# Kernel optimization log

Measured on AMD Instinct MI355X. Metric: run time of the kernel, lower is better.

The kernel has to match this reference:

```python
import jax, jax.numpy as jnp
import numpy as np

PAD = 0          # pad_token_id == blank_index in the source module
NEG = -1e30      # log-space 'zero' (safe for fp32)


def _ctc_mean_loss(labels, logits, logits_mask):
    """Faithful jnp port of CTCLoss.call: tf.nn.ctc_loss (alpha forward DP,
    blank=pad, dense labels, logits [B,T,V]) + feasibility mask + mean."""
    B, T, V = logits.shape
    L = labels.shape[1]
    S = 2 * L + 1

    labels_len = jnp.sum(labels != PAD, axis=-1).astype(jnp.int32)   # [B]
    logits_len = jnp.sum(logits_mask, axis=-1).astype(jnp.int32)     # [B]

    logp = jax.nn.log_softmax(logits.astype(jnp.float32), axis=-1)   # [B,T,V]

    # Blank-interleaved extended label sequence: (blank, l1, blank, l2, ..., blank)
    ext = jnp.full((B, S), PAD, dtype=labels.dtype)
    ext = ext.at[:, 1::2].set(labels)                                # [B,S]
    ext_m2 = jnp.pad(ext, ((0, 0), (2, 0)), constant_values=PAD)[:, :S]
    allow_skip = (ext != PAD) & (ext != ext_m2)                      # [B,S]

    # Emission log-probs gathered at extended labels: em[b,t,s] = logp[b,t,ext[b,s]]
    em = jnp.take_along_axis(logp, jnp.broadcast_to(ext[:, None, :], (B, T, S)), axis=2)
    em = em.transpose(1, 0, 2)                                       # [T,B,S]

    neg = jnp.float32(NEG)
    alpha0 = jnp.full((B, S), neg, dtype=jnp.float32)
    alpha0 = alpha0.at[:, 0].set(em[0, :, 0]).at[:, 1].set(em[0, :, 1])

    t_idx = jnp.arange(1, T, dtype=jnp.int32)
    active = t_idx[:, None] < logits_len[None, :]                    # [T-1,B]

    def step(alpha, inp):
        em_t, act = inp                                              # [B,S], [B]
        p1 = jnp.concatenate([jnp.full((B, 1), neg), alpha[:, :-1]], axis=1)
        p2 = jnp.concatenate([jnp.full((B, 2), neg), alpha[:, :-2]], axis=1)
        p2 = jnp.where(allow_skip, p2, neg)
        new = em_t + jnp.logaddexp(jnp.logaddexp(alpha, p1), p2)
        alpha = jnp.where(act[:, None], new, alpha)                  # freeze past logit_len
        return alpha, None

    alpha, _ = jax.lax.scan(step, alpha0, (em[1:], active))          # [B,S]

    e = 2 * labels_len                                               # end of extended seq
    a_end = jnp.take_along_axis(alpha, e[:, None], axis=1)[:, 0]
    a_end1 = jnp.take_along_axis(alpha, jnp.maximum(e - 1, 0)[:, None], axis=1)[:, 0]
    loss = -jnp.logaddexp(a_end, a_end1)                             # per-example NLL

    loss_mask = (labels_len <= logits_len).astype(jnp.float32)
    return jnp.mean(loss * loss_mask)


def setup_inputs() -> dict:
    key = jax.random.key(0)
    k1, k2, k3, k4 = jax.random.split(key, 4)
    B, T, V, L = 256, 1024, 64, 64

    lab_len = jax.random.randint(k1, (B,), L // 2, L + 1)            # [32,64]
    vals = jax.random.randint(k2, (B, L), 1, V)                      # non-blank tokens
    labels = jnp.where(jnp.arange(L)[None, :] < lab_len[:, None], vals, 0).astype(jnp.int64)

    log_len = jax.random.randint(k3, (B,), 2 * L + 64, T + 1)        # feasible alignments
    logits_mask = jnp.arange(T)[None, :] < log_len[:, None]          # prefix-True mask

    logits = jax.random.normal(k4, (B, T, V), dtype=jnp.float32)
    return {"labels": labels, "logits": logits, "logits_mask": logits_mask}


def reference(labels, logits, logits_mask):
    return _ctc_mean_loss(labels, logits, logits_mask)
```

## Files before the change

### kernel.cpp

```cpp
#include <hip/hip_runtime.h>

#define BB 256
#define TT 1024
#define VV 64
#define LL 64
#define LOG2E 1.4426950408889634f
#define LN2   0.6931471805599453f

__device__ __forceinline__ int   f2i(float x) { return __float_as_int(x); }
__device__ __forceinline__ float i2f(int x)   { return __int_as_float(x); }

__device__ __forceinline__ float wave_max63(float x) {
  x = fmaxf(x, i2f(__builtin_amdgcn_update_dpp(0, f2i(x), 0x111, 0xF, 0xF, true)));
  x = fmaxf(x, i2f(__builtin_amdgcn_update_dpp(0, f2i(x), 0x112, 0xF, 0xF, true)));
  x = fmaxf(x, i2f(__builtin_amdgcn_update_dpp(0, f2i(x), 0x114, 0xF, 0xF, true)));
  x = fmaxf(x, i2f(__builtin_amdgcn_update_dpp(0, f2i(x), 0x118, 0xF, 0xF, true)));
  x = fmaxf(x, i2f(__builtin_amdgcn_update_dpp(0, f2i(x), 0x142, 0xF, 0xF, true)));
  x = fmaxf(x, i2f(__builtin_amdgcn_update_dpp(0, f2i(x), 0x143, 0xF, 0xF, true)));
  return i2f(__builtin_amdgcn_readlane(f2i(x), 63));
}

extern "C" __global__ void __launch_bounds__(320, 1)
ctc_fused(const int* __restrict__ labels, const float* __restrict__ logits,
          const int* __restrict__ mask, float* __restrict__ out) {
  __shared__ float lsePart[4];
  const int b = blockIdx.x;
  const int tid = threadIdx.x;
  const int lane = tid & 63;
  const int wv = tid >> 6;

  const float* lg = logits + (size_t)b * TT * VV;

  int lsum = 0;
  const int* mrow = mask + b * TT;
#pragma unroll
  for (int k = 0; k < TT / 64; ++k) lsum += mrow[lane + (k << 6)];
#pragma unroll
  for (int off = 32; off; off >>= 1) lsum += __shfl_xor(lsum, off);
  int len = __builtin_amdgcn_readfirstlane(lsum);
  len = len < 1 ? 1 : (len > TT ? TT : len);
  const int nwin = (len + 15) >> 4;

  int lab_len = 0;
  float A0 = 0.0f, A1 = 0.0f, A2 = 0.0f;
  int ctot = 0;

#define RENORM() { \
    const float mxv = wave_max63(fmaxf(fmaxf(A0, A1), A2)); \
    const int eb_ = (f2i(mxv) >> 23) & 255; \
    int kk = (eb_ > 0 && eb_ < 255) ? (187 - eb_) : 0; \
    kk = kk > 126 ? 126 : (kk < -126 ? -126 : kk); \
    ctot += kk; \
    const float sc = i2f((127 + kk) << 23); \
    A0 *= sc; A1 *= sc; A2 *= sc; \
  }

#define STEPU(U) { \
    const float A1p = i2f(__builtin_amdgcn_update_dpp(0, f2i(A1), 0x138, 0xF, 0xF, false)); \
    const float nA0 = c##U * (A0 + A1p); \
    const float nA1 = g##U * fmaf(sk, A1p, A0 + A1); \
    A2 = c##U * (A2 + A1); \
    A0 = nA0; A1 = nA1; \
  }

#define STEPM(U) { \
    const float A1p = i2f(__builtin_amdgcn_update_dpp(0, f2i(A1), 0x138, 0xF, 0xF, false)); \
    const float nA0 = c##U * (A0 + A1p); \
    const float nA1 = g##U * fmaf(sk, A1p, A0 + A1); \
    const float nA2 = c##U * (A2 + A1); \
    const bool act = (tbase + (U)) < len; \
    A0 = act ? nA0 : A0; A1 = act ? nA1 : A1; A2 = act ? nA2 : A2; \
  }

  if (wv == 0) {
    const int lab = labels[b * LL + lane] & 63;
    lab_len = (int)__popcll(__ballot(lab != 0));
    const int plab = __builtin_amdgcn_update_dpp(0, lab, 0x138, 0xF, 0xF, false);
    const float sk = (lab != 0 && lab != plab) ? 1.0f : 0.0f;
    A0 = (lane == 0) ? 1.0f : 0.0f;
    __builtin_amdgcn_s_setprio(1);

    const int cu = lane & 15;
    const float* lgg = lg + lab;
    const float* lgc = lg + (cu << 6);

    float qa_c, qb_c, qc_c;
    float qa_g0, qa_g1, qa_g2, qa_g3, qa_g4, qa_g5, qa_g6, qa_g7,
          qa_g8, qa_g9, qa_g10, qa_g11, qa_g12, qa_g13, qa_g14, qa_g15;
    float qb_g0, qb_g1, qb_g2, qb_g3, qb_g4, qb_g5, qb_g6, qb_g7,
          qb_g8, qb_g9, qb_g10, qb_g11, qb_g12, qb_g13, qb_g14, qb_g15;
    float qc_g0, qc_g1, qc_g2, qc_g3, qc_g4, qc_g5, qc_g6, qc_g7,
          qc_g8, qc_g9, qc_g10, qc_g11, qc_g12, qc_g13, qc_g14, qc_g15;

#define CISSUE(WN, S) { \
    const float* pg_ = lgg + ((WN) << 10); \
    S##_g0  = pg_[0];    S##_g1  = pg_[64];   S##_g2  = pg_[128];  S##_g3  = pg_[192]; \
    S##_g4  = pg_[256];  S##_g5  = pg_[320];  S##_g6  = pg_[384];  S##_g7  = pg_[448]; \
    S##_g8  = pg_[512];  S##_g9  = pg_[576];  S##_g10 = pg_[640];  S##_g11 = pg_[704]; \
    S##_g12 = pg_[768];  S##_g13 = pg_[832];  S##_g14 = pg_[896];  S##_g15 = pg_[960]; \
    S##_c = lgc[(WN) << 10]; \
  }

#define CBODY(W, S) { \
    const float cv = __builtin_amdgcn_exp2f(S##_c * LOG2E); \
    const float g0  = __builtin_amdgcn_exp2f(S##_g0  * LOG2E); \
    const float g1  = __builtin_amdgcn_exp2f(S##_g1  * LOG2E); \
    const float g2  = __builtin_amdgcn_exp2f(S##_g2  * LOG2E); \
    const float g3  = __builtin_amdgcn_exp2f(S##_g3  * LOG2E); \
    const float g4  = __builtin_amdgcn_exp2f(S##_g4  * LOG2E); \
    const float g5  = __builtin_amdgcn_exp2f(S##_g5  * LOG2E); \
    const float g6  = __builtin_amdgcn_exp2f(S##_g6  * LOG2E); \
    const float g7  = __builtin_amdgcn_exp2f(S##_g7  * LOG2E); \
    const float g8  = __builtin_amdgcn_exp2f(S##_g8  * LOG2E); \
    const float g9  = __builtin_amdgcn_exp2f(S##_g9  * LOG2E); \
    const float g10 = __builtin_amdgcn_exp2f(S##_g10 * LOG2E); \
    const float g11 = __builtin_amdgcn_exp2f(S##_g11 * LOG2E); \
    const float g12 = __builtin_amdgcn_exp2f(S##_g12 * LOG2E); \
    const float g13 = __builtin_amdgcn_exp2f(S##_g13 * LOG2E); \
    const float g14 = __builtin_amdgcn_exp2f(S##_g14 * LOG2E); \
    const float g15 = __builtin_amdgcn_exp2f(S##_g15 * LOG2E); \
    if ((W) + 3 < 64) { CISSUE((W) + 3, S) }   \
    const float c0  = i2f(__builtin_amdgcn_readlane(f2i(cv), 0)); \
    const float c1  = i2f(__builtin_amdgcn_readlane(f2i(cv), 1)); \
    const float c2  = i2f(__builtin_amdgcn_readlane(f2i(cv), 2)); \
    const float c3  = i2f(__builtin_amdgcn_readlane(f2i(cv), 3)); \
    const float c4  = i2f(__builtin_amdgcn_readlane(f2i(cv), 4)); \
    const float c5  = i2f(__builtin_amdgcn_readlane(f2i(cv), 5)); \
    const float c6  = i2f(__builtin_amdgcn_readlane(f2i(cv), 6)); \
    const float c7  = i2f(__builtin_amdgcn_readlane(f2i(cv), 7)); \
    const float c8  = i2f(__builtin_amdgcn_readlane(f2i(cv), 8)); \
    const float c9  = i2f(__builtin_amdgcn_readlane(f2i(cv), 9)); \
    const float c10 = i2f(__builtin_amdgcn_readlane(f2i(cv), 10)); \
    const float c11 = i2f(__builtin_amdgcn_readlane(f2i(cv), 11)); \
    const float c12 = i2f(__builtin_amdgcn_readlane(f2i(cv), 12)); \
    const float c13 = i2f(__builtin_amdgcn_readlane(f2i(cv), 13)); \
    const float c14 = i2f(__builtin_amdgcn_readlane(f2i(cv), 14)); \
    const float c15 = i2f(__builtin_amdgcn_readlane(f2i(cv), 15)); \
    RENORM() \
    const int tbase = (W) << 4; \
    if (tbase + 16 <= len) { \
      STEPU(0)  STEPU(1)  STEPU(2)  STEPU(3)  STEPU(4)  STEPU(5)  STEPU(6)  STEPU(7) \
      STEPU(8)  STEPU(9)  STEPU(10) STEPU(11) STEPU(12) STEPU(13) STEPU(14) STEPU(15) \
    } else { \
      STEPM(0)  STEPM(1)  STEPM(2)  STEPM(3)  STEPM(4)  STEPM(5)  STEPM(6)  STEPM(7) \
      STEPM(8)  STEPM(9)  STEPM(10) STEPM(11) STEPM(12) STEPM(13) STEPM(14) STEPM(15) \
    } \
  }

    CISSUE(0, qa) CISSUE(1, qb) CISSUE(2, qc)
    int w = 0;
    for (; w + 3 <= nwin; w += 3) {
      CBODY(w, qa) CBODY(w + 1, qb) CBODY(w + 2, qc)
    }
    if (w < nwin) { CBODY(w, qa) ++w; }
    if (w < nwin) { CBODY(w, qb) ++w; }
#undef CBODY
#undef CISSUE
  } else {
    const int prow = lane >> 4;
    const int pcol = (lane & 15) << 2;
    const float* pb_ = lg + (((((wv - 1) << 2) + prow) << 6) + pcol);
    float acc = 0.0f;
    float4 pa, pb, pc;

#define LISSUE(K, S) { S = *(const float4*)(pb_ + ((K) << 10)); }

#define LBODY(K, S) { \
    const float e0 = __builtin_amdgcn_exp2f(S.x * LOG2E); \
    const float e1 = __builtin_amdgcn_exp2f(S.y * LOG2E); \
    const float e2 = __builtin_amdgcn_exp2f(S.z * LOG2E); \
    const float e3 = __builtin_amdgcn_exp2f(S.w * LOG2E); \
    if ((K) + 3 < 64) { LISSUE((K) + 3, S) } \
    float s = (e0 + e1) + (e2 + e3); \
    s += i2f(__builtin_amdgcn_update_dpp(0, f2i(s), 0x111, 0xF, 0xF, true)); \
    s += i2f(__builtin_amdgcn_update_dpp(0, f2i(s), 0x112, 0xF, 0xF, true)); \
    s += i2f(__builtin_amdgcn_update_dpp(0, f2i(s), 0x114, 0xF, 0xF, true)); \
    s += i2f(__builtin_amdgcn_update_dpp(0, f2i(s), 0x118, 0xF, 0xF, true)); \
    if ((lane & 15) == 15 && ((((K) << 4) + ((wv - 1) << 2) + prow) < len)) acc += __logf(s); \
  }

    LISSUE(0, pa) LISSUE(1, pb) LISSUE(2, pc)
    int k = 0;
    for (; k + 3 <= nwin; k += 3) {
      LBODY(k, pa) LBODY(k + 1, pb) LBODY(k + 2, pc)
    }
    if (k < nwin) { LBODY(k, pa) ++k; }
    if (k < nwin) { LBODY(k, pb) ++k; }
#undef LBODY
#undef LISSUE

    float a = ((lane & 15) == 15) ? acc : 0.0f;
    a += __shfl_xor(a, 16);
    a += __shfl_xor(a, 32);
    if (lane == 63) lsePart[wv - 1] = a;
    asm volatile("s_waitcnt lgkmcnt(0)");
  }

  asm volatile("s_waitcnt vmcnt(0)");
  __builtin_amdgcn_s_barrier();

  if (wv == 0) {
    float ae, ae1;
    if (lab_len >= LL) {
      ae  = i2f(__builtin_amdgcn_readlane(f2i(A2), 63));
      ae1 = i2f(__builtin_amdgcn_readlane(f2i(A1), 63));
    } else if (lab_len >= 1) {
      ae  = i2f(__builtin_amdgcn_readlane(f2i(A0), lab_len));
      ae1 = i2f(__builtin_amdgcn_readlane(f2i(A1), lab_len - 1));
    } else {
      ae  = i2f(__builtin_amdgcn_readlane(f2i(A0), 0));
      ae1 = ae;
    }
    const float se = ae + ae1;
    float loss = ((lsePart[0] + lsePart[1]) + (lsePart[2] + lsePart[3]))
               - LN2 * (__builtin_amdgcn_logf(se) - (float)ctot);
    if (lab_len > len) loss = 0.0f;
    if (lane == 0) atomicAdd(out, loss * (1.0f / 256.0f));
  }
#undef STEPM
#undef STEPU
#undef RENORM
}

extern "C" void kernel_launch(void* const* d_in, const int* in_sizes, int n_in,
                              void* d_out, int out_size, void* d_ws, size_t ws_size,
                              hipStream_t stream) {
  (void)in_sizes; (void)n_in; (void)out_size; (void)d_ws; (void)ws_size;
  hipMemsetAsync(d_out, 0, sizeof(float), stream);
  ctc_fused<<<dim3(BB), dim3(320), 0, stream>>>(
      (const int*)d_in[0], (const float*)d_in[1], (const int*)d_in[2], (float*)d_out);
}
```

Before: 126.5 us.

## Split CTC recursion into forward-alpha and backward-beta waves meeting at midpoint

Result: faster. 119.6 us (-5.4%).

```diff
diff --git a/kernel.cpp b/kernel.cpp
--- a/kernel.cpp
+++ b/kernel.cpp
@@ -20,10 +20,13 @@
   return i2f(__builtin_amdgcn_readlane(f2i(x), 63));
 }
 
-extern "C" __global__ void __launch_bounds__(320, 1)
+extern "C" __global__ void __launch_bounds__(384, 1)
 ctc_fused(const int* __restrict__ labels, const float* __restrict__ logits,
           const int* __restrict__ mask, float* __restrict__ out) {
   __shared__ float lsePart[4];
+  __shared__ float sG0v[64], sG1v[64];
+  __shared__ float sG2s;
+  __shared__ int   sCtB;
   const int b = blockIdx.x;
   const int tid = threadIdx.x;
   const int lane = tid & 63;
@@ -40,36 +43,32 @@
   int len = __builtin_amdgcn_readfirstlane(lsum);
   len = len < 1 ? 1 : (len > TT ? TT : len);
   const int nwin = (len + 15) >> 4;
+  int mid = len >> 1; mid = mid < 1 ? 1 : mid;
+  const int nwF = (mid + 15) >> 4;
+  const int nwB = (len - mid + 15) >> 4;
 
   int lab_len = 0;
   float A0 = 0.0f, A1 = 0.0f, A2 = 0.0f;
-  int ctot = 0;
-
-#define RENORM() { \
-    const float mxv = wave_max63(fmaxf(fmaxf(A0, A1), A2)); \
+  int ctotA = 0;
+
+#define RENORM3(X, Y, Z, CT) { \
+    const float mxv = wave_max63(fmaxf(fmaxf(X, Y), Z)); \
     const int eb_ = (f2i(mxv) >> 23) & 255; \
     int kk = (eb_ > 0 && eb_ < 255) ? (187 - eb_) : 0; \
     kk = kk > 126 ? 126 : (kk < -126 ? -126 : kk); \
-    ctot += kk; \
+    CT += kk; \
     const float sc = i2f((127 + kk) << 23); \
-    A0 *= sc; A1 *= sc; A2 *= sc; \
-  }
-
-#define STEPU(U) { \
-    const float A1p = i2f(__builtin_amdgcn_update_dpp(0, f2i(A1), 0x138, 0xF, 0xF, false)); \
-    const float nA0 = c##U * (A0 + A1p); \
-    const float nA1 = g##U * fmaf(sk, A1p, A0 + A1); \
-    A2 = c##U * (A2 + A1); \
-    A0 = nA0; A1 = nA1; \
-  }
-
-#define STEPM(U) { \
-    const float A1p = i2f(__builtin_amdgcn_update_dpp(0, f2i(A1), 0x138, 0xF, 0xF, false)); \
-    const float nA0 = c##U * (A0 + A1p); \
-    const float nA1 = g##U * fmaf(sk, A1p, A0 + A1); \
-    const float nA2 = c##U * (A2 + A1); \
-    const bool act = (tbase + (U)) < len; \
-    A0 = act ? nA0 : A0; A1 = act ? nA1 : A1; A2 = act ? nA2 : A2; \
+    X *= sc; Y *= sc; Z *= sc; \
+  }
+
+#define RESCALE45(X, Y, Z, CT) { \
+    const float mxv = wave_max63(fmaxf(fmaxf(X, Y), Z)); \
+    const int eb_ = (f2i(mxv) >> 23) & 255; \
+    int kk = (eb_ > 0 && eb_ < 255) ? (172 - eb_) : 0; \
+    kk = kk > 126 ? 126 : (kk < -126 ? -126 : kk); \
+    CT += kk; \
+    const float sc = i2f((127 + kk) << 23); \
+    X *= sc; Y *= sc; Z *= sc; \
   }
 
   if (wv == 0) {
@@ -92,7 +91,7 @@
     float qc_g0, qc_g1, qc_g2, qc_g3, qc_g4, qc_g5, qc_g6, qc_g7,
           qc_g8, qc_g9, qc_g10, qc_g11, qc_g12, qc_g13, qc_g14, qc_g15;
 
-#define CISSUE(WN, S) { \
+#define FISSUE(WN, S) { \
     const float* pg_ = lgg + ((WN) << 10); \
     S##_g0  = pg_[0];    S##_g1  = pg_[64];   S##_g2  = pg_[128];  S##_g3  = pg_[192]; \
     S##_g4  = pg_[256];  S##_g5  = pg_[320];  S##_g6  = pg_[384];  S##_g7  = pg_[448]; \
@@ -101,7 +100,24 @@
     S##_c = lgc[(WN) << 10]; \
   }
 
-#define CBODY(W, S) { \
+#define FSTEPU(U) { \
+    const float A1p = i2f(__builtin_amdgcn_update_dpp(0, f2i(A1), 0x138, 0xF, 0xF, false)); \
+    const float nA0 = c##U * (A0 + A1p); \
+    const float nA1 = g##U * fmaf(sk, A1p, A0 + A1); \
+    A2 = c##U * (A2 + A1); \
+    A0 = nA0; A1 = nA1; \
+  }
+
+#define FSTEPM(U) { \
+    const float A1p = i2f(__builtin_amdgcn_update_dpp(0, f2i(A1), 0x138, 0xF, 0xF, false)); \
+    const float nA0 = c##U * (A0 + A1p); \
+    const float nA1 = g##U * fmaf(sk, A1p, A0 + A1); \
+    const float nA2 = c##U * (A2 + A1); \
+    const bool act = (tbase + (U)) < mid; \
+    A0 = act ? nA0 : A0; A1 = act ? nA1 : A1; A2 = act ? nA2 : A2; \
+  }
+
+#define FBODY(W, S) { \
     const float cv = __builtin_amdgcn_exp2f(S##_c * LOG2E); \
     const float g0  = __builtin_amdgcn_exp2f(S##_g0  * LOG2E); \
     const float g1  = __builtin_amdgcn_exp2f(S##_g1  * LOG2E); \
@@ -119,7 +135,7 @@
     const float g13 = __builtin_amdgcn_exp2f(S##_g13 * LOG2E); \
     const float g14 = __builtin_amdgcn_exp2f(S##_g14 * LOG2E); \
     const float g15 = __builtin_amdgcn_exp2f(S##_g15 * LOG2E); \
-    if ((W) + 3 < 64) { CISSUE((W) + 3, S) }   \
+    if ((W) + 3 < 64) { FISSUE((W) + 3, S) } \
     const float c0  = i2f(__builtin_amdgcn_readlane(f2i(cv), 0)); \
     const float c1  = i2f(__builtin_amdgcn_readlane(f2i(cv), 1)); \
     const float c2  = i2f(__builtin_amdgcn_readlane(f2i(cv), 2)); \
@@ -136,30 +152,157 @@
     const float c13 = i2f(__builtin_amdgcn_readlane(f2i(cv), 13)); \
     const float c14 = i2f(__builtin_amdgcn_readlane(f2i(cv), 14)); \
     const float c15 = i2f(__builtin_amdgcn_readlane(f2i(cv), 15)); \
-    RENORM() \
+    RENORM3(A0, A1, A2, ctotA) \
     const int tbase = (W) << 4; \
-    if (tbase + 16 <= len) { \
-      STEPU(0)  STEPU(1)  STEPU(2)  STEPU(3)  STEPU(4)  STEPU(5)  STEPU(6)  STEPU(7) \
-      STEPU(8)  STEPU(9)  STEPU(10) STEPU(11) STEPU(12) STEPU(13) STEPU(14) STEPU(15) \
+    if (tbase + 16 <= mid) { \
+      FSTEPU(0)  FSTEPU(1)  FSTEPU(2)  FSTEPU(3)  FSTEPU(4)  FSTEPU(5)  FSTEPU(6)  FSTEPU(7) \
+      FSTEPU(8)  FSTEPU(9)  FSTEPU(10) FSTEPU(11) FSTEPU(12) FSTEPU(13) FSTEPU(14) FSTEPU(15) \
     } else { \
-      STEPM(0)  STEPM(1)  STEPM(2)  STEPM(3)  STEPM(4)  STEPM(5)  STEPM(6)  STEPM(7) \
-      STEPM(8)  STEPM(9)  STEPM(10) STEPM(11) STEPM(12) STEPM(13) STEPM(14) STEPM(15) \
+      FSTEPM(0)  FSTEPM(1)  FSTEPM(2)  FSTEPM(3)  FSTEPM(4)  FSTEPM(5)  FSTEPM(6)  FSTEPM(7) \
+      FSTEPM(8)  FSTEPM(9)  FSTEPM(10) FSTEPM(11) FSTEPM(12) FSTEPM(13) FSTEPM(14) FSTEPM(15) \
     } \
   }
 
-    CISSUE(0, qa) CISSUE(1, qb) CISSUE(2, qc)
+    FISSUE(0, qa) FISSUE(1, qb) FISSUE(2, qc)
     int w = 0;
-    for (; w + 3 <= nwin; w += 3) {
-      CBODY(w, qa) CBODY(w + 1, qb) CBODY(w + 2, qc)
+    for (; w + 3 <= nwF; w += 3) {
+      FBODY(w, qa) FBODY(w + 1, qb) FBODY(w + 2, qc)
     }
-    if (w < nwin) { CBODY(w, qa) ++w; }
-    if (w < nwin) { CBODY(w, qb) ++w; }
-#undef CBODY
-#undef CISSUE
+    if (w < nwF) { FBODY(w, qa) ++w; }
+    if (w < nwF) { FBODY(w, qb) ++w; }
+#undef FBODY
+#undef FSTEPM
+#undef FSTEPU
+#undef FISSUE
+    RESCALE45(A0, A1, A2, ctotA)
+
+  } else if (wv == 1) {
+    const int lab = labels[b * LL + lane] & 63;
+    const int ll = (int)__popcll(__ballot(lab != 0));
+    const int plab = __builtin_amdgcn_update_dpp(0, lab, 0x138, 0xF, 0xF, false);
+    const float sk = (lab != 0 && lab != plab) ? 1.0f : 0.0f;
+    const float skp = i2f(__builtin_amdgcn_update_dpp(0, f2i(sk), 0x130, 0xF, 0xF, false));
+    const bool is63 = (lane == 63);
+    __builtin_amdgcn_s_setprio(1);
+
+    float G0 = 0.0f, G1 = 0.0f, G2 = 0.0f;
+    if (ll == 0)            { G0 = (lane == 0) ? 2.0f : 0.0f; }
+    else if (ll >= LL)      { G2 = 1.0f; G1 = is63 ? 1.0f : 0.0f; }
+    else {
+      G0 = (lane == ll) ? 1.0f : 0.0f;
+      G1 = (lane == ll - 1) ? 1.0f : 0.0f;
+    }
+    int ctotB = 0;
+
+    const int cu = lane & 15;
+    const float* lgg = lg + lab;
+
+    float ra_c, rb_c, rc_c;
+    float ra_g0, ra_g1, ra_g2, ra_g3, ra_g4, ra_g5, ra_g6, ra_g7,
+          ra_g8, ra_g9, ra_g10, ra_g11, ra_g12, ra_g13, ra_g14, ra_g15;
+    float rb_g0, rb_g1, rb_g2, rb_g3, rb_g4, rb_g5, rb_g6, rb_g7,
+          rb_g8, rb_g9, rb_g10, rb_g11, rb_g12, rb_g13, rb_g14, rb_g15;
+    float rc_g0, rc_g1, rc_g2, rc_g3, rc_g4, rc_g5, rc_g6, rc_g7,
+          rc_g8, rc_g9, rc_g10, rc_g11, rc_g12, rc_g13, rc_g14, rc_g15;
+
+#define BLD(RW) ( (RW) < 0 ? 0 : (RW) )
+#define BISSUE(J, S) { \
+    const int br_ = len - 1 - ((J) << 4); \
+    S##_g0  = lgg[BLD(br_ - 0)  << 6]; S##_g1  = lgg[BLD(br_ - 1)  << 6]; \
+    S##_g2  = lgg[BLD(br_ - 2)  << 6]; S##_g3  = lgg[BLD(br_ - 3)  << 6]; \
+    S##_g4  = lgg[BLD(br_ - 4)  << 6]; S##_g5  = lgg[BLD(br_ - 5)  << 6]; \
+    S##_g6  = lgg[BLD(br_ - 6)  << 6]; S##_g7  = lgg[BLD(br_ - 7)  << 6]; \
+    S##_g8  = lgg[BLD(br_ - 8)  << 6]; S##_g9  = lgg[BLD(br_ - 9)  << 6]; \
+    S##_g10 = lgg[BLD(br_ - 10) << 6]; S##_g11 = lgg[BLD(br_ - 11) << 6]; \
+    S##_g12 = lgg[BLD(br_ - 12) << 6]; S##_g13 = lgg[BLD(br_ - 13) << 6]; \
+    S##_g14 = lgg[BLD(br_ - 14) << 6]; S##_g15 = lgg[BLD(br_ - 15) << 6]; \
+    S##_c = lg[BLD(br_ - cu) << 6]; \
+  }
+
+#define BSTEPU(U) { \
+    const float V_ = i2f(__builtin_amdgcn_update_dpp(0, f2i(G1), 0x130, 0xF, 0xF, false)); \
+    float U_ = i2f(__builtin_amdgcn_update_dpp(0, f2i(G0), 0x130, 0xF, 0xF, false)); \
+    U_ = is63 ? G2 : U_; \
+    const float nG0 = fmaf(cB##U, G0, gB##U * G1); \
+    const float nG1 = fmaf(gB##U, G1, fmaf(cB##U, U_, hB##U * V_)); \
+    G2 = cB##U * G2; \
+    G0 = nG0; G1 = nG1; \
+  }
+
+#define BSTEPM(U) { \
+    const float V_ = i2f(__builtin_amdgcn_update_dpp(0, f2i(G1), 0x130, 0xF, 0xF, false)); \
+    float U_ = i2f(__builtin_amdgcn_update_dpp(0, f2i(G0), 0x130, 0xF, 0xF, false)); \
+    U_ = is63 ? G2 : U_; \
+    const float nG0 = fmaf(cB##U, G0, gB##U * G1); \
+    const float nG1 = fmaf(gB##U, G1, fmaf(cB##U, U_, hB##U * V_)); \
+    const float nG2 = cB##U * G2; \
+    const bool act = (brow0 - (U)) >= mid; \
+    G0 = act ? nG0 : G0; G1 = act ? nG1 : G1; G2 = act ? nG2 : G2; \
+  }
+
+#define BPREP(U, S) \
+    const float gB##U = __builtin_amdgcn_exp2f(S##_g##U * LOG2E); \
+    const float hB##U = skp * i2f(__builtin_amdgcn_update_dpp(0, f2i(gB##U), 0x130, 0xF, 0xF, false));
+
+#define BBODY(J, S) { \
+    const int brow0 = len - 1 - ((J) << 4); \
+    const float cv = __builtin_amdgcn_exp2f(S##_c * LOG2E); \
+    BPREP(0, S)  BPREP(1, S)  BPREP(2, S)  BPREP(3, S) \
+    BPREP(4, S)  BPREP(5, S)  BPREP(6, S)  BPREP(7, S) \
+    BPREP(8, S)  BPREP(9, S)  BPREP(10, S) BPREP(11, S) \
+    BPREP(12, S) BPREP(13, S) BPREP(14, S) BPREP(15, S) \
+    if ((J) + 3 < 64) { BISSUE((J) + 3, S) } \
+    const float cB0  = i2f(__builtin_amdgcn_readlane(f2i(cv), 0)); \
+    const float cB1  = i2f(__builtin_amdgcn_readlane(f2i(cv), 1)); \
+    const float cB2  = i2f(__builtin_amdgcn_readlane(f2i(cv), 2)); \
+    const float cB3  = i2f(__builtin_amdgcn_readlane(f2i(cv), 3)); \
+    const float cB4  = i2f(__builtin_amdgcn_readlane(f2i(cv), 4)); \
+    const float cB5  = i2f(__builtin_amdgcn_readlane(f2i(cv), 5)); \
+    const float cB6  = i2f(__builtin_amdgcn_readlane(f2i(cv), 6)); \
+    const float cB7  = i2f(__builtin_amdgcn_readlane(f2i(cv), 7)); \
+    const float cB8  = i2f(__builtin_amdgcn_readlane(f2i(cv), 8)); \
+    const float cB9  = i2f(__builtin_amdgcn_readlane(f2i(cv), 9)); \
+    const float cB10 = i2f(__builtin_amdgcn_readlane(f2i(cv), 10)); \
+    const float cB11 = i2f(__builtin_amdgcn_readlane(f2i(cv), 11)); \
+    const float cB12 = i2f(__builtin_amdgcn_readlane(f2i(cv), 12)); \
+    const float cB13 = i2f(__builtin_amdgcn_readlane(f2i(cv), 13)); \
+    const float cB14 = i2f(__builtin_amdgcn_readlane(f2i(cv), 14)); \
+    const float cB15 = i2f(__builtin_amdgcn_readlane(f2i(cv), 15)); \
+    RENORM3(G0, G1, G2, ctotB) \
+    if (brow0 - 15 >= mid) { \
+      BSTEPU(0)  BSTEPU(1)  BSTEPU(2)  BSTEPU(3)  BSTEPU(4)  BSTEPU(5)  BSTEPU(6)  BSTEPU(7) \
+      BSTEPU(8)  BSTEPU(9)  BSTEPU(10) BSTEPU(11) BSTEPU(12) BSTEPU(13) BSTEPU(14) BSTEPU(15) \
+    } else { \
+      BSTEPM(0)  BSTEPM(1)  BSTEPM(2)  BSTEPM(3)  BSTEPM(4)  BSTEPM(5)  BSTEPM(6)  BSTEPM(7) \
+      BSTEPM(8)  BSTEPM(9)  BSTEPM(10) BSTEPM(11) BSTEPM(12) BSTEPM(13) BSTEPM(14) BSTEPM(15) \
+    } \
+  }
+
+    BISSUE(0, ra) BISSUE(1, rb) BISSUE(2, rc)
+    int j = 0;
+    for (; j + 3 <= nwB; j += 3) {
+      BBODY(j, ra) BBODY(j + 1, rb) BBODY(j + 2, rc)
+    }
+    if (j < nwB) { BBODY(j, ra) ++j; }
+    if (j < nwB) { BBODY(j, rb) ++j; }
+#undef BBODY
+#undef BPREP
+#undef BSTEPM
+#undef BSTEPU
+#undef BISSUE
+#undef BLD
+    RESCALE45(G0, G1, G2, ctotB)
+
+    sG0v[lane] = G0;
+    sG1v[lane] = G1;
+    if (is63) sG2s = G2;
+    if (lane == 0) sCtB = ctotB;
+
   } else {
+    const int pw = wv - 2;
     const int prow = lane >> 4;
     const int pcol = (lane & 15) << 2;
-    const float* pb_ = lg + (((((wv - 1) << 2) + prow) << 6) + pcol);
+    const float* pb_ = lg + ((((pw << 2) + prow) << 6) + pcol);
     float acc = 0.0f;
     float4 pa, pb, pc;
 
@@ -176,7 +319,7 @@
     s += i2f(__builtin_amdgcn_update_dpp(0, f2i(s), 0x112, 0xF, 0xF, true)); \
     s += i2f(__builtin_amdgcn_update_dpp(0, f2i(s), 0x114, 0xF, 0xF, true)); \
     s += i2f(__builtin_amdgcn_update_dpp(0, f2i(s), 0x118, 0xF, 0xF, true)); \
-    if ((lane & 15) == 15 && ((((K) << 4) + ((wv - 1) << 2) + prow) < len)) acc += __logf(s); \
+    if ((lane & 15) == 15 && ((((K) << 4) + (pw << 2) + prow) < len)) acc += __logf(s); \
   }
 
     LISSUE(0, pa) LISSUE(1, pb) LISSUE(2, pc)
@@ -192,34 +335,24 @@
     float a = ((lane & 15) == 15) ? acc : 0.0f;
     a += __shfl_xor(a, 16);
     a += __shfl_xor(a, 32);
-    if (lane == 63) lsePart[wv - 1] = a;
-    asm volatile("s_waitcnt lgkmcnt(0)");
-  }
-
-  asm volatile("s_waitcnt vmcnt(0)");
-  __builtin_amdgcn_s_barrier();
+    if (lane == 63) lsePart[pw] = a;
+  }
+
+  __syncthreads();
 
   if (wv == 0) {
-    float ae, ae1;
-    if (lab_len >= LL) {
-      ae  = i2f(__builtin_amdgcn_readlane(f2i(A2), 63));
-      ae1 = i2f(__builtin_amdgcn_readlane(f2i(A1), 63));
-    } else if (lab_len >= 1) {
-      ae  = i2f(__builtin_amdgcn_readlane(f2i(A0), lab_len));
-      ae1 = i2f(__builtin_amdgcn_readlane(f2i(A1), lab_len - 1));
-    } else {
-      ae  = i2f(__builtin_amdgcn_readlane(f2i(A0), 0));
-      ae1 = ae;
-    }
-    const float se = ae + ae1;
+    float prod = A0 * sG0v[lane] + A1 * sG1v[lane];
+    if (lane == 63) prod = fmaf(A2, sG2s, prod);
+#pragma unroll
+    for (int off = 32; off; off >>= 1) prod += __shfl_xor(prod, off);
+    const float p = fmaxf(prod, 1e-37f);
     float loss = ((lsePart[0] + lsePart[1]) + (lsePart[2] + lsePart[3]))
-               - LN2 * (__builtin_amdgcn_logf(se) - (float)ctot);
+               - LN2 * (__builtin_amdgcn_logf(p) - (float)(ctotA + sCtB));
     if (lab_len > len) loss = 0.0f;
     if (lane == 0) atomicAdd(out, loss * (1.0f / 256.0f));
   }
-#undef STEPM
-#undef STEPU
-#undef RENORM
+#undef RESCALE45
+#undef RENORM3
 }
 
 extern "C" void kernel_launch(void* const* d_in, const int* in_sizes, int n_in,
@@ -227,6 +360,6 @@
                               hipStream_t stream) {
   (void)in_sizes; (void)n_in; (void)out_size; (void)d_ws; (void)ws_size;
   hipMemsetAsync(d_out, 0, sizeof(float), stream);
-  ctc_fused<<<dim3(BB), dim3(320), 0, stream>>>(
+  ctc_fused<<<dim3(BB), dim3(384), 0, stream>>>(
       (const int*)d_in[0], (const float*)d_in[1], (const int*)d_in[2], (float*)d_out);
 }
```

## Split CTC alpha recursion into forward and backward halves meeting at midpoint

Applied to the files above, without the earlier changes.

Result: faster. 112.5 us (-11.1%).

```diff
diff --git a/kernel.cpp b/kernel.cpp
--- a/kernel.cpp
+++ b/kernel.cpp
@@ -20,10 +20,13 @@
   return i2f(__builtin_amdgcn_readlane(f2i(x), 63));
 }
 
-extern "C" __global__ void __launch_bounds__(320, 1)
+extern "C" __global__ void __launch_bounds__(384, 1)
 ctc_fused(const int* __restrict__ labels, const float* __restrict__ logits,
           const int* __restrict__ mask, float* __restrict__ out) {
   __shared__ float lsePart[4];
+  __shared__ float sG0v[64], sG1v[64];
+  __shared__ float sG2s;
+  __shared__ int   sCtB;
   const int b = blockIdx.x;
   const int tid = threadIdx.x;
   const int lane = tid & 63;
@@ -40,22 +43,36 @@
   int len = __builtin_amdgcn_readfirstlane(lsum);
   len = len < 1 ? 1 : (len > TT ? TT : len);
   const int nwin = (len + 15) >> 4;
+  int mid = len >> 1; mid = mid < 1 ? 1 : mid;
+  const int nwF = (mid + 15) >> 4;
+  const int lenB = len - mid;
+  const int nwB = (lenB + 15) >> 4;
 
   int lab_len = 0;
-  float A0 = 0.0f, A1 = 0.0f, A2 = 0.0f;
-  int ctot = 0;
-
-#define RENORM() { \
-    const float mxv = wave_max63(fmaxf(fmaxf(A0, A1), A2)); \
+  float Ab0 = 0.0f, Ab1 = 0.0f, Ab2 = 0.0f;
+  int ctotA = 0;
+
+#define RENORM3(X, Y, Z, CT) { \
+    const float mxv = wave_max63(fmaxf(fmaxf(X, Y), Z)); \
     const int eb_ = (f2i(mxv) >> 23) & 255; \
     int kk = (eb_ > 0 && eb_ < 255) ? (187 - eb_) : 0; \
     kk = kk > 126 ? 126 : (kk < -126 ? -126 : kk); \
-    ctot += kk; \
+    CT += kk; \
     const float sc = i2f((127 + kk) << 23); \
-    A0 *= sc; A1 *= sc; A2 *= sc; \
-  }
-
-#define STEPU(U) { \
+    X *= sc; Y *= sc; Z *= sc; \
+  }
+
+#define RESCALE45(X, Y, Z, CT) { \
+    const float mxv = wave_max63(fmaxf(fmaxf(X, Y), Z)); \
+    const int eb_ = (f2i(mxv) >> 23) & 255; \
+    int kk = (eb_ > 0 && eb_ < 255) ? (172 - eb_) : 0; \
+    kk = kk > 126 ? 126 : (kk < -126 ? -126 : kk); \
+    CT += kk; \
+    const float sc = i2f((127 + kk) << 23); \
+    X *= sc; Y *= sc; Z *= sc; \
+  }
+
+#define DPSTEPU(U) { \
     const float A1p = i2f(__builtin_amdgcn_update_dpp(0, f2i(A1), 0x138, 0xF, 0xF, false)); \
     const float nA0 = c##U * (A0 + A1p); \
     const float nA1 = g##U * fmaf(sk, A1p, A0 + A1); \
@@ -63,45 +80,16 @@
     A0 = nA0; A1 = nA1; \
   }
 
-#define STEPM(U) { \
+#define DPSTEPM(U, BOUND) { \
     const float A1p = i2f(__builtin_amdgcn_update_dpp(0, f2i(A1), 0x138, 0xF, 0xF, false)); \
     const float nA0 = c##U * (A0 + A1p); \
     const float nA1 = g##U * fmaf(sk, A1p, A0 + A1); \
     const float nA2 = c##U * (A2 + A1); \
-    const bool act = (tbase + (U)) < len; \
+    const bool act = (tbase + (U)) < (BOUND); \
     A0 = act ? nA0 : A0; A1 = act ? nA1 : A1; A2 = act ? nA2 : A2; \
   }
 
-  if (wv == 0) {
-    const int lab = labels[b * LL + lane] & 63;
-    lab_len = (int)__popcll(__ballot(lab != 0));
-    const int plab = __builtin_amdgcn_update_dpp(0, lab, 0x138, 0xF, 0xF, false);
-    const float sk = (lab != 0 && lab != plab) ? 1.0f : 0.0f;
-    A0 = (lane == 0) ? 1.0f : 0.0f;
-    __builtin_amdgcn_s_setprio(1);
-
-    const int cu = lane & 15;
-    const float* lgg = lg + lab;
-    const float* lgc = lg + (cu << 6);
-
-    float qa_c, qb_c, qc_c;
-    float qa_g0, qa_g1, qa_g2, qa_g3, qa_g4, qa_g5, qa_g6, qa_g7,
-          qa_g8, qa_g9, qa_g10, qa_g11, qa_g12, qa_g13, qa_g14, qa_g15;
-    float qb_g0, qb_g1, qb_g2, qb_g3, qb_g4, qb_g5, qb_g6, qb_g7,
-          qb_g8, qb_g9, qb_g10, qb_g11, qb_g12, qb_g13, qb_g14, qb_g15;
-    float qc_g0, qc_g1, qc_g2, qc_g3, qc_g4, qc_g5, qc_g6, qc_g7,
-          qc_g8, qc_g9, qc_g10, qc_g11, qc_g12, qc_g13, qc_g14, qc_g15;
-
-#define CISSUE(WN, S) { \
-    const float* pg_ = lgg + ((WN) << 10); \
-    S##_g0  = pg_[0];    S##_g1  = pg_[64];   S##_g2  = pg_[128];  S##_g3  = pg_[192]; \
-    S##_g4  = pg_[256];  S##_g5  = pg_[320];  S##_g6  = pg_[384];  S##_g7  = pg_[448]; \
-    S##_g8  = pg_[512];  S##_g9  = pg_[576];  S##_g10 = pg_[640];  S##_g11 = pg_[704]; \
-    S##_g12 = pg_[768];  S##_g13 = pg_[832];  S##_g14 = pg_[896];  S##_g15 = pg_[960]; \
-    S##_c = lgc[(WN) << 10]; \
-  }
-
-#define CBODY(W, S) { \
+#define DPBODY(W, S, PREF, BOUND, CT) { \
     const float cv = __builtin_amdgcn_exp2f(S##_c * LOG2E); \
     const float g0  = __builtin_amdgcn_exp2f(S##_g0  * LOG2E); \
     const float g1  = __builtin_amdgcn_exp2f(S##_g1  * LOG2E); \
@@ -119,7 +107,7 @@
     const float g13 = __builtin_amdgcn_exp2f(S##_g13 * LOG2E); \
     const float g14 = __builtin_amdgcn_exp2f(S##_g14 * LOG2E); \
     const float g15 = __builtin_amdgcn_exp2f(S##_g15 * LOG2E); \
-    if ((W) + 3 < 64) { CISSUE((W) + 3, S) }   \
+    PREF \
     const float c0  = i2f(__builtin_amdgcn_readlane(f2i(cv), 0)); \
     const float c1  = i2f(__builtin_amdgcn_readlane(f2i(cv), 1)); \
     const float c2  = i2f(__builtin_amdgcn_readlane(f2i(cv), 2)); \
@@ -136,30 +124,124 @@
     const float c13 = i2f(__builtin_amdgcn_readlane(f2i(cv), 13)); \
     const float c14 = i2f(__builtin_amdgcn_readlane(f2i(cv), 14)); \
     const float c15 = i2f(__builtin_amdgcn_readlane(f2i(cv), 15)); \
-    RENORM() \
+    RENORM3(A0, A1, A2, CT) \
     const int tbase = (W) << 4; \
-    if (tbase + 16 <= len) { \
-      STEPU(0)  STEPU(1)  STEPU(2)  STEPU(3)  STEPU(4)  STEPU(5)  STEPU(6)  STEPU(7) \
-      STEPU(8)  STEPU(9)  STEPU(10) STEPU(11) STEPU(12) STEPU(13) STEPU(14) STEPU(15) \
+    if (tbase + 16 <= (BOUND)) { \
+      DPSTEPU(0)  DPSTEPU(1)  DPSTEPU(2)  DPSTEPU(3) \
+      DPSTEPU(4)  DPSTEPU(5)  DPSTEPU(6)  DPSTEPU(7) \
+      DPSTEPU(8)  DPSTEPU(9)  DPSTEPU(10) DPSTEPU(11) \
+      DPSTEPU(12) DPSTEPU(13) DPSTEPU(14) DPSTEPU(15) \
     } else { \
-      STEPM(0)  STEPM(1)  STEPM(2)  STEPM(3)  STEPM(4)  STEPM(5)  STEPM(6)  STEPM(7) \
-      STEPM(8)  STEPM(9)  STEPM(10) STEPM(11) STEPM(12) STEPM(13) STEPM(14) STEPM(15) \
+      DPSTEPM(0, BOUND)  DPSTEPM(1, BOUND)  DPSTEPM(2, BOUND)  DPSTEPM(3, BOUND) \
+      DPSTEPM(4, BOUND)  DPSTEPM(5, BOUND)  DPSTEPM(6, BOUND)  DPSTEPM(7, BOUND) \
+      DPSTEPM(8, BOUND)  DPSTEPM(9, BOUND)  DPSTEPM(10, BOUND) DPSTEPM(11, BOUND) \
+      DPSTEPM(12, BOUND) DPSTEPM(13, BOUND) DPSTEPM(14, BOUND) DPSTEPM(15, BOUND) \
     } \
   }
 
-    CISSUE(0, qa) CISSUE(1, qb) CISSUE(2, qc)
+  if (wv == 0) {
+    const int lab = labels[b * LL + lane] & 63;
+    lab_len = (int)__popcll(__ballot(lab != 0));
+    const int plab = __builtin_amdgcn_update_dpp(0, lab, 0x138, 0xF, 0xF, false);
+    const float sk = (lab != 0 && lab != plab) ? 1.0f : 0.0f;
+    float A0 = (lane == 0) ? 1.0f : 0.0f;
+    float A1 = 0.0f, A2 = 0.0f;
+    __builtin_amdgcn_s_setprio(1);
+
+    const int cu = lane & 15;
+    const float* lgg = lg + lab;
+    const float* lgc = lg + (cu << 6);
+
+    float qa_c, qb_c, qc_c;
+    float qa_g0, qa_g1, qa_g2, qa_g3, qa_g4, qa_g5, qa_g6, qa_g7,
+          qa_g8, qa_g9, qa_g10, qa_g11, qa_g12, qa_g13, qa_g14, qa_g15;
+    float qb_g0, qb_g1, qb_g2, qb_g3, qb_g4, qb_g5, qb_g6, qb_g7,
+          qb_g8, qb_g9, qb_g10, qb_g11, qb_g12, qb_g13, qb_g14, qb_g15;
+    float qc_g0, qc_g1, qc_g2, qc_g3, qc_g4, qc_g5, qc_g6, qc_g7,
+          qc_g8, qc_g9, qc_g10, qc_g11, qc_g12, qc_g13, qc_g14, qc_g15;
+
+#define FISSUE(WN, S) { \
+    const float* pg_ = lgg + ((WN) << 10); \
+    S##_g0  = pg_[0];    S##_g1  = pg_[64];   S##_g2  = pg_[128];  S##_g3  = pg_[192]; \
+    S##_g4  = pg_[256];  S##_g5  = pg_[320];  S##_g6  = pg_[384];  S##_g7  = pg_[448]; \
+    S##_g8  = pg_[512];  S##_g9  = pg_[576];  S##_g10 = pg_[640];  S##_g11 = pg_[704]; \
+    S##_g12 = pg_[768];  S##_g13 = pg_[832];  S##_g14 = pg_[896];  S##_g15 = pg_[960]; \
+    S##_c = lgc[(WN) << 10]; \
+  }
+
+    FISSUE(0, qa) FISSUE(1, qb) FISSUE(2, qc)
     int w = 0;
-    for (; w + 3 <= nwin; w += 3) {
-      CBODY(w, qa) CBODY(w + 1, qb) CBODY(w + 2, qc)
+    for (; w + 3 <= nwF; w += 3) {
+      DPBODY(w,     qa, { if (w + 3 < 64) { FISSUE(w + 3, qa) } }, mid, ctotA)
+      DPBODY(w + 1, qb, { if (w + 4 < 64) { FISSUE(w + 4, qb) } }, mid, ctotA)
+      DPBODY(w + 2, qc, { if (w + 5 < 64) { FISSUE(w + 5, qc) } }, mid, ctotA)
     }
-    if (w < nwin) { CBODY(w, qa) ++w; }
-    if (w < nwin) { CBODY(w, qb) ++w; }
-#undef CBODY
-#undef CISSUE
+    if (w < nwF) { DPBODY(w, qa, { if (w + 3 < 64) { FISSUE(w + 3, qa) } }, mid, ctotA) ++w; }
+    if (w < nwF) { DPBODY(w, qb, { if (w + 3 < 64) { FISSUE(w + 3, qb) } }, mid, ctotA) ++w; }
+#undef FISSUE
+    RESCALE45(A0, A1, A2, ctotA)
+    const float A1p = i2f(__builtin_amdgcn_update_dpp(0, f2i(A1), 0x138, 0xF, 0xF, false));
+    Ab0 = A0 + A1p;
+    Ab1 = fmaf(sk, A1p, A0 + A1);
+    Ab2 = A2 + A1;
+
+  } else if (wv == 1) {
+    const int lab0 = labels[b * LL + lane] & 63;
+    const int ll = (int)__popcll(__ballot(lab0 != 0));
+    int rlab = 0;
+    if (lane < ll) rlab = labels[b * LL + (ll - 1 - lane)] & 63;
+    const int plab = __builtin_amdgcn_update_dpp(0, rlab, 0x138, 0xF, 0xF, false);
+    const float sk = (rlab != 0 && rlab != plab) ? 1.0f : 0.0f;
+    float A0 = (lane == 0) ? (ll == 0 ? 2.0f : 1.0f) : 0.0f;
+    float A1 = 0.0f, A2 = 0.0f;
+    int ctotB = 0;
+    __builtin_amdgcn_s_setprio(1);
+
+    const int cu = lane & 15;
+    const float* lgg = lg + rlab;
+    const int lenm1 = len - 1;
+
+    float qa_c, qb_c, qc_c;
+    float qa_g0, qa_g1, qa_g2, qa_g3, qa_g4, qa_g5, qa_g6, qa_g7,
+          qa_g8, qa_g9, qa_g10, qa_g11, qa_g12, qa_g13, qa_g14, qa_g15;
+    float qb_g0, qb_g1, qb_g2, qb_g3, qb_g4, qb_g5, qb_g6, qb_g7,
+          qb_g8, qb_g9, qb_g10, qb_g11, qb_g12, qb_g13, qb_g14, qb_g15;
+    float qc_g0, qc_g1, qc_g2, qc_g3, qc_g4, qc_g5, qc_g6, qc_g7,
+          qc_g8, qc_g9, qc_g10, qc_g11, qc_g12, qc_g13, qc_g14, qc_g15;
+
+#define RISSUE(WN, S) { \
+    int br_ = lenm1 - ((WN) << 4); \
+    br_ = br_ < 15 ? 15 : br_; \
+    const float* pg_ = lgg + ((size_t)br_ << 6); \
+    S##_g0  = pg_[0];     S##_g1  = pg_[-64];   S##_g2  = pg_[-128];  S##_g3  = pg_[-192]; \
+    S##_g4  = pg_[-256];  S##_g5  = pg_[-320];  S##_g6  = pg_[-384];  S##_g7  = pg_[-448]; \
+    S##_g8  = pg_[-512];  S##_g9  = pg_[-576];  S##_g10 = pg_[-640];  S##_g11 = pg_[-704]; \
+    S##_g12 = pg_[-768];  S##_g13 = pg_[-832];  S##_g14 = pg_[-896];  S##_g15 = pg_[-960]; \
+    S##_c = lg[(br_ - cu) << 6]; \
+  }
+
+    RISSUE(0, qa) RISSUE(1, qb) RISSUE(2, qc)
+    int w = 0;
+    for (; w + 3 <= nwB; w += 3) {
+      DPBODY(w,     qa, { RISSUE(w + 3, qa) }, lenB, ctotB)
+      DPBODY(w + 1, qb, { RISSUE(w + 4, qb) }, lenB, ctotB)
+      DPBODY(w + 2, qc, { RISSUE(w + 5, qc) }, lenB, ctotB)
+    }
+    if (w < nwB) { DPBODY(w, qa, { RISSUE(w + 3, qa) }, lenB, ctotB) ++w; }
+    if (w < nwB) { DPBODY(w, qb, { RISSUE(w + 3, qb) }, lenB, ctotB) ++w; }
+#undef RISSUE
+    RESCALE45(A0, A1, A2, ctotB)
+
+    sG0v[lane] = A0;
+    sG1v[lane] = A1;
+    if (lane == 63) sG2s = A2;
+    if (lane == 0) sCtB = ctotB;
+
   } else {
+    const int pw = wv - 2;
     const int prow = lane >> 4;
     const int pcol = (lane & 15) << 2;
-    const float* pb_ = lg + (((((wv - 1) << 2) + prow) << 6) + pcol);
+    const float* pb_ = lg + ((((pw << 2) + prow) << 6) + pcol);
     float acc = 0.0f;
     float4 pa, pb, pc;
 
@@ -176,7 +258,7 @@
     s += i2f(__builtin_amdgcn_update_dpp(0, f2i(s), 0x112, 0xF, 0xF, true)); \
     s += i2f(__builtin_amdgcn_update_dpp(0, f2i(s), 0x114, 0xF, 0xF, true)); \
     s += i2f(__builtin_amdgcn_update_dpp(0, f2i(s), 0x118, 0xF, 0xF, true)); \
-    if ((lane & 15) == 15 && ((((K) << 4) + ((wv - 1) << 2) + prow) < len)) acc += __logf(s); \
+    if ((lane & 15) == 15 && ((((K) << 4) + (pw << 2) + prow) < len)) acc += __logf(s); \
   }
 
     LISSUE(0, pa) LISSUE(1, pb) LISSUE(2, pc)
@@ -192,34 +274,34 @@
     float a = ((lane & 15) == 15) ? acc : 0.0f;
     a += __shfl_xor(a, 16);
     a += __shfl_xor(a, 32);
-    if (lane == 63) lsePart[wv - 1] = a;
-    asm volatile("s_waitcnt lgkmcnt(0)");
-  }
-
-  asm volatile("s_waitcnt vmcnt(0)");
-  __builtin_amdgcn_s_barrier();
+    if (lane == 63) lsePart[pw] = a;
+  }
+
+  __syncthreads();
 
   if (wv == 0) {
-    float ae, ae1;
-    if (lab_len >= LL) {
-      ae  = i2f(__builtin_amdgcn_readlane(f2i(A2), 63));
-      ae1 = i2f(__builtin_amdgcn_readlane(f2i(A1), 63));
-    } else if (lab_len >= 1) {
-      ae  = i2f(__builtin_amdgcn_readlane(f2i(A0), lab_len));
-      ae1 = i2f(__builtin_amdgcn_readlane(f2i(A1), lab_len - 1));
-    } else {
-      ae  = i2f(__builtin_amdgcn_readlane(f2i(A0), 0));
-      ae1 = ae;
-    }
-    const float se = ae + ae1;
+    const int llv = lab_len;
+    const int i0 = llv - lane;
+    const int i1 = llv - 1 - lane;
+    float t0 = 0.0f;
+    if (i0 >= 0 && i0 < 64) t0 = sG0v[i0];
+    else if (i0 == 64)      t0 = sG2s;
+    const float t1 = (i1 >= 0) ? sG1v[i1] : 0.0f;
+    float prod = Ab0 * t0 + Ab1 * t1;
+    if (lane == 63 && llv == 64) prod = fmaf(Ab2, sG0v[0], prod);
+#pragma unroll
+    for (int off = 32; off; off >>= 1) prod += __shfl_xor(prod, off);
+    const float p = fmaxf(prod, 1e-37f);
     float loss = ((lsePart[0] + lsePart[1]) + (lsePart[2] + lsePart[3]))
-               - LN2 * (__builtin_amdgcn_logf(se) - (float)ctot);
+               - LN2 * (__builtin_amdgcn_logf(p) - (float)(ctotA + sCtB));
     if (lab_len > len) loss = 0.0f;
     if (lane == 0) atomicAdd(out, loss * (1.0f / 256.0f));
   }
-#undef STEPM
-#undef STEPU
-#undef RENORM
+#undef DPBODY
+#undef DPSTEPM
+#undef DPSTEPU
+#undef RESCALE45
+#undef RENORM3
 }
 
 extern "C" void kernel_launch(void* const* d_in, const int* in_sizes, int n_in,
@@ -227,6 +309,6 @@
                               hipStream_t stream) {
   (void)in_sizes; (void)n_in; (void)out_size; (void)d_ws; (void)ws_size;
   hipMemsetAsync(d_out, 0, sizeof(float), stream);
-  ctc_fused<<<dim3(BB), dim3(320), 0, stream>>>(
+  ctc_fused<<<dim3(BB), dim3(384), 0, stream>>>(
       (const int*)d_in[0], (const float*)d_in[1], (const int*)d_in[2], (float*)d_out);
 }
```
